# Kernel tuning notes

Measured on AMD Instinct MI355X. Metric: run time of the kernel, lower is better.

The kernel has to match this reference:

```python
import jax, jax.numpy as jnp
import numpy as np

D_MODEL = 1024
M = 64            # oscillators; state dim N = 2*M
N = 2 * M
N_H = 2           # Householder reflections per step
DT = 0.1
OMEGA_MAX = 100.0
BATCH, SEQ = 8, 2048


def setup_inputs() -> dict:
    key = jax.random.key(0)
    ks = jax.random.split(key, 8)
    u = jax.random.normal(ks[0], (BATCH, SEQ, D_MODEL), jnp.float32)
    # learned parameters (scaled like the module's small-gain init)
    W_A = jax.random.normal(ks[1], (M, D_MODEL), jnp.float32) * 0.01
    b_A = jnp.zeros((M,), jnp.float32)
    W_k = jax.random.normal(ks[2], (N_H, N, D_MODEL), jnp.float32) * 0.02
    b_k = jnp.zeros((N_H, N), jnp.float32)
    W_beta = jax.random.normal(ks[3], (N_H, D_MODEL), jnp.float32) * 0.02
    b_beta = jnp.zeros((N_H,), jnp.float32)
    B_w = jax.random.normal(ks[4], (N, D_MODEL), jnp.float32) * 0.02
    B_b = jnp.zeros((N,), jnp.float32)
    C = jax.random.normal(ks[5], (D_MODEL, N), jnp.float32) * 0.01
    D = jax.random.normal(ks[6], (D_MODEL,), jnp.float32) * 0.01
    return dict(u=u, W_A=W_A, b_A=b_A, W_k=W_k, b_k=b_k,
                W_beta=W_beta, b_beta=b_beta, B_w=B_w, B_b=B_b, C=C, D=D)


def reference(u, W_A, b_A, W_k, b_k, W_beta, b_beta, B_w, B_b, C, D):
    batch = u.shape[0]
    # --- precompute all input-dependent per-step quantities as big GEMMs ---
    A = jax.nn.relu(jnp.einsum('btd,md->btm', u, W_A) + b_A)
    A = jnp.minimum(A, OMEGA_MAX)                       # clamp(max=omega_max)
    S = 1.0 / (1.0 + (DT * DT) * A)                     # (B,T,M)
    K = jnp.einsum('btd,jnd->btjn', u, W_k) + b_k       # (B,T,n_h,N)
    K = K / jnp.maximum(jnp.linalg.norm(K, axis=-1, keepdims=True), 1e-12)
    beta = 2.0 * jax.nn.sigmoid(jnp.einsum('btd,jd->btj', u, W_beta) + b_beta)
    Bt = jnp.einsum('btd,nd->btn', u, B_w) + B_b        # (B,T,N)

    # time-major for scan
    xs = (jnp.moveaxis(A, 1, 0), jnp.moveaxis(S, 1, 0), jnp.moveaxis(K, 1, 0),
          jnp.moveaxis(beta, 1, 0), jnp.moveaxis(Bt, 1, 0))
    h0 = jnp.zeros((batch, N), u.dtype)

    def step(h, x):
        A_t, S_t, K_t, beta_t, B_t = x
        # oscillatory rotation-contraction R_t @ h (m 2x2 blocks)
        z, y = h[:, :M], h[:, M:]
        z_new = S_t * z - DT * A_t * S_t * y
        y_new = DT * S_t * z + S_t * y
        h = jnp.concatenate([z_new, y_new], axis=-1)
        # sequential Householder product H_t @ h (fixed small n_h loop)
        for j in range(N_H):
            k = K_t[:, j]                                # (B,N), unit norm
            dot = jnp.sum(k * h, axis=-1, keepdims=True)
            h = h - beta_t[:, j:j + 1] * k * dot
        h = h + B_t
        return h, h

    _, hs = jax.lax.scan(step, h0, xs)                  # (T,B,N)
    hs = jnp.moveaxis(hs, 0, 1)                         # (B,T,N)
    return jnp.einsum('btn,dn->btd', hs, C) + u * D
```

## Files before the change

kernel.cpp:

```cpp
#include <hip/hip_runtime.h>
#include <cmath>


#define NTOK 16384
#define TT 2048
#define BB 8
#define DM 1024
#define FS 520
#define CH 32
#define LCH 64
#define NW 448
#define NWP 512

typedef short bf16x8 __attribute__((ext_vector_type(8)));
typedef float f32x4 __attribute__((ext_vector_type(4)));

#define GLOAD_LDS16(g, l)                                          \
  __builtin_amdgcn_global_load_lds(                                \
      (const __attribute__((address_space(1))) void*)(g),          \
      (__attribute__((address_space(3))) void*)(l), 16, 0, 0)

__global__ __launch_bounds__(256) void packW(
    const float* __restrict__ W_A, const float* __restrict__ b_A,
    const float* __restrict__ W_k, const float* __restrict__ b_k,
    const float* __restrict__ b_beta,
    const float* __restrict__ B_w, const float* __restrict__ B_b,
    float* __restrict__ Wp, float* __restrict__ bias) {
  int r = blockIdx.x;
  int tid = threadIdx.x;
  const float* src;
  float bv;
  if (r < 64)       { src = W_A + (size_t)r * DM;         bv = b_A[r]; }
  else if (r < 320) { src = W_k + (size_t)(r - 64) * DM;  bv = b_k[r - 64]; }
  else              { src = B_w + (size_t)(r - 320) * DM; bv = B_b[r - 320]; }
  ((float4*)(Wp + (size_t)r * DM))[tid] = ((const float4*)src)[tid];
  if (tid == 0) bias[r] = bv;
  if (r == 0 && tid < 2) bias[448 + tid] = b_beta[tid];
}

__global__ __launch_bounds__(256) void transK(
    const float* __restrict__ src, float* __restrict__ dst, int M, int N) {
  __shared__ float tile[64][68];
  const int m0 = blockIdx.x * 64, n0 = blockIdx.y * 64;
  const int tid = threadIdx.x;
#pragma unroll
  for (int l = 0; l < 4; ++l) {
    int idx = tid + l * 256;
    int r = idx >> 4, c4 = (idx & 15) * 4;
    float4 v = *(const float4*)(src + (size_t)(m0 + r) * N + n0 + c4);
    tile[r][c4 + 0] = v.x; tile[r][c4 + 1] = v.y;
    tile[r][c4 + 2] = v.z; tile[r][c4 + 3] = v.w;
  }
  __syncthreads();
#pragma unroll
  for (int l = 0; l < 4; ++l) {
    int idx = tid + l * 256;
    int c = idx >> 4, r4 = (idx & 15) * 4;
    float4 w = make_float4(tile[r4 + 0][c], tile[r4 + 1][c],
                           tile[r4 + 2][c], tile[r4 + 3][c]);
    *(float4*)(dst + (size_t)(n0 + c) * M + m0 + r4) = w;
  }
}

__device__ inline unsigned short bf16_rne(float x) {
  unsigned b = __float_as_uint(x);
  b += 0x7FFFu + ((b >> 16) & 1u);
  return (unsigned short)(b >> 16);
}

__device__ inline void split_bf16(float x, unsigned short& h, unsigned short& l) {
  unsigned b = __float_as_uint(x);
  h = (unsigned short)(b >> 16);
  float rem = x - __uint_as_float(b & 0xFFFF0000u);
  l = bf16_rne(rem);
}

__global__ __launch_bounds__(256) void convertU(
    const float* __restrict__ u, unsigned short* __restrict__ uh,
    unsigned short* __restrict__ ul) {
  int gid = blockIdx.x * 256 + threadIdx.x;
  int m = gid >> 8;
  int g = gid & 255;
  float4 v = *(const float4*)(u + (size_t)m * DM + g * 4);
  int kt = g >> 3, gg = g & 7;
  int p = gg & 3, h = gg >> 2;
  int mr = m & 127, mb = m >> 7;
  int pp = p ^ ((mr >> 2) & 3);
  size_t dst = ((size_t)(mb * 32 + kt)) * 4096 + mr * 32 + ((pp << 1) | h) * 4;
  ushort4 hi, lo;
  split_bf16(v.x, hi.x, lo.x);
  split_bf16(v.y, hi.y, lo.y);
  split_bf16(v.z, hi.z, lo.z);
  split_bf16(v.w, hi.w, lo.w);
  *(ushort4*)(uh + dst) = hi;
  *(ushort4*)(ul + dst) = lo;
}

__global__ __launch_bounds__(256) void convertW(
    const float* __restrict__ Wp, unsigned short* __restrict__ Wb) {
  int gid = blockIdx.x * 256 + threadIdx.x;
  int n = gid >> 8, g = gid & 255;
  int kt = g >> 3, gg = g & 7;
  int p = gg & 3, h = gg >> 2;
  int nr = n & 127, nb = n >> 7;
  int pp = p ^ ((nr >> 2) & 3);
  size_t dst = ((size_t)(nb * 32 + kt)) * 4096 + nr * 32 + ((pp << 1) | h) * 4;
  ushort4 hv = make_ushort4(0, 0, 0, 0);
  if (n < NW) {
    float4 v = *(const float4*)(Wp + (size_t)n * DM + g * 4);
    hv.x = bf16_rne(v.x); hv.y = bf16_rne(v.y);
    hv.z = bf16_rne(v.z); hv.w = bf16_rne(v.w);
  }
  *(ushort4*)(Wb + dst) = hv;
}

__global__ __launch_bounds__(256) void convertC(
    const float* __restrict__ Cm, unsigned short* __restrict__ Chp,
    unsigned short* __restrict__ Clp) {
  int gid = blockIdx.x * 256 + threadIdx.x;
  int d = gid >> 5;
  int g = gid & 31;
  float4 v = *(const float4*)(Cm + (size_t)d * 128 + g * 4);
  int kt = g >> 3, gg = g & 7;
  int p = gg & 3, h = gg >> 2;
  int nr = d & 127, nb = d >> 7;
  int pp = p ^ ((nr >> 2) & 3);
  size_t dst = ((size_t)(nb * 4 + kt)) * 4096 + nr * 32 + ((pp << 1) | h) * 4;
  ushort4 hi, lo;
  split_bf16(v.x, hi.x, lo.x);
  split_bf16(v.y, hi.y, lo.y);
  split_bf16(v.z, hi.z, lo.z);
  split_bf16(v.w, hi.w, lo.w);
  *(ushort4*)(Chp + dst) = hi;
  *(ushort4*)(Clp + dst) = lo;
}

__global__ __launch_bounds__(256) void gemmA_mfma(
    const unsigned short* __restrict__ uh, const unsigned short* __restrict__ ul,
    const unsigned short* __restrict__ Wb, float* __restrict__ Feat, int npass) {
  __shared__ __align__(16) unsigned short As[4096];
  __shared__ __align__(16) unsigned short Bs[4096];
  const int tid = threadIdx.x;
  const int wv = tid >> 6, ln = tid & 63;
  const int lr = ln & 15, G = ln >> 4;
  const int wm = wv >> 1, wn = wv & 1;
  const int x = G ^ (lr >> 2);
  f32x4 acc[4][4];
#pragma unroll
  for (int i = 0; i < 4; ++i)
#pragma unroll
    for (int j = 0; j < 4; ++j) acc[i][j] = (f32x4){0.f, 0.f, 0.f, 0.f};

  const size_t aBase = (size_t)blockIdx.x * 32 * 4096;
  const size_t bBase = (size_t)blockIdx.y * 32 * 4096;
  const int so = wv * 512 + ln * 8;
  const int ld = wv * 512;

  for (int pass = 0; pass < npass; ++pass) {
    const unsigned short* ua = pass ? ul : uh;
    for (int kt = 0; kt < 32; ++kt) {
      const unsigned short* ga = ua + aBase + (size_t)kt * 4096;
      const unsigned short* gb = Wb + bBase + (size_t)kt * 4096;
      GLOAD_LDS16(ga + so,        As + ld);
      GLOAD_LDS16(ga + 2048 + so, As + 2048 + ld);
      GLOAD_LDS16(gb + so,        Bs + ld);
      GLOAD_LDS16(gb + 2048 + so, Bs + 2048 + ld);
      __syncthreads();
      bf16x8 af[4], bfr[4];
      const char* Ab = (const char*)As + ((wm * 64 + lr) << 6) + (x << 4);
      const char* Bb = (const char*)Bs + ((wn * 64 + lr) << 6) + (x << 4);
#pragma unroll
      for (int i = 0; i < 4; ++i) {
        af[i]  = *(const bf16x8*)(Ab + i * 1024);
        bfr[i] = *(const bf16x8*)(Bb + i * 1024);
      }
#pragma unroll
      for (int i = 0; i < 4; ++i)
#pragma unroll
        for (int j = 0; j < 4; ++j)
          acc[i][j] = __builtin_amdgcn_mfma_f32_16x16x32_bf16(
              af[i], bfr[j], acc[i][j], 0, 0, 0);
      __syncthreads();
    }
  }
  const int row0 = (blockIdx.x << 7) + wm * 64 + (G << 2);
  const int col0 = (blockIdx.y << 7) + wn * 64 + lr;
  float* fb = Feat + (size_t)row0 * FS + col0;
#pragma unroll
  for (int i = 0; i < 4; ++i)
#pragma unroll
    for (int j = 0; j < 4; ++j) {
      float* d = fb + (size_t)(i * 16) * FS + j * 16;
#pragma unroll
      for (int r = 0; r < 4; ++r) d[(size_t)r * FS] = acc[i][j][r];
    }
}

__global__ __launch_bounds__(256) void gemmC_mfma(
    const unsigned short* __restrict__ hsh, const unsigned short* __restrict__ hsl,
    const unsigned short* __restrict__ Chp, const unsigned short* __restrict__ Clp,
    const float* __restrict__ u, const float* __restrict__ Dv,
    float* __restrict__ out) {
  __shared__ __align__(16) unsigned short As[4096];
  __shared__ __align__(16) unsigned short Bs[4096];
  const int tid = threadIdx.x;
  const int wv = tid >> 6, ln = tid & 63;
  const int lr = ln & 15, G = ln >> 4;
  const int wm = wv >> 1, wn = wv & 1;
  const int x = G ^ (lr >> 2);
  f32x4 acc[4][4];
#pragma unroll
  for (int i = 0; i < 4; ++i)
#pragma unroll
    for (int j = 0; j < 4; ++j) acc[i][j] = (f32x4){0.f, 0.f, 0.f, 0.f};

  const size_t aBase = (size_t)blockIdx.x * 4 * 4096;
  const size_t bBase = (size_t)blockIdx.y * 4 * 4096;
  const int so = wv * 512 + ln * 8;
  const int ld = wv * 512;

#pragma unroll 1
  for (int pass = 0; pass < 3; ++pass) {
    const unsigned short* pa = (pass == 1) ? hsl : hsh;
    const unsigned short* pb = (pass == 2) ? Clp : Chp;
#pragma unroll 1
    for (int kt = 0; kt < 4; ++kt) {
      const unsigned short* ga = pa + aBase + (size_t)kt * 4096;
      const unsigned short* gb = pb + bBase + (size_t)kt * 4096;
      GLOAD_LDS16(ga + so,        As + ld);
      GLOAD_LDS16(ga + 2048 + so, As + 2048 + ld);
      GLOAD_LDS16(gb + so,        Bs + ld);
      GLOAD_LDS16(gb + 2048 + so, Bs + 2048 + ld);
      __syncthreads();
      bf16x8 af[4], bfr[4];
      const char* Ab = (const char*)As + ((wm * 64 + lr) << 6) + (x << 4);
      const char* Bb = (const char*)Bs + ((wn * 64 + lr) << 6) + (x << 4);
#pragma unroll
      for (int i = 0; i < 4; ++i) {
        af[i]  = *(const bf16x8*)(Ab + i * 1024);
        bfr[i] = *(const bf16x8*)(Bb + i * 1024);
      }
#pragma unroll
      for (int i = 0; i < 4; ++i)
#pragma unroll
        for (int j = 0; j < 4; ++j)
          acc[i][j] = __builtin_amdgcn_mfma_f32_16x16x32_bf16(
              af[i], bfr[j], acc[i][j], 0, 0, 0);
      __syncthreads();
    }
  }
  const int row0 = (blockIdx.x << 7) + wm * 64 + (G << 2);
  const int col0 = (blockIdx.y << 7) + wn * 64 + lr;
#pragma unroll
  for (int j = 0; j < 4; ++j) {
    float dv = Dv[col0 + j * 16];
#pragma unroll
    for (int i = 0; i < 4; ++i) {
#pragma unroll
      for (int r = 0; r < 4; ++r) {
        size_t off = (size_t)(row0 + i * 16 + r) * DM + col0 + j * 16;
        out[off] = fmaf(u[off], dv, acc[i][j][r]);
      }
    }
  }
}

__global__ __launch_bounds__(256) void gemmA_f32(
    const float* __restrict__ u, const float* __restrict__ WpT,
    float* __restrict__ Feat) {
  __shared__ float us2[128][36];
  __shared__ float wsm[32][68];
  const int tid = threadIdx.x;
  const int tx = tid & 15, ty = tid >> 4;
  const int m0 = blockIdx.x * 128;
  const int n0 = blockIdx.y * 64;
  float acc[8][4];
#pragma unroll
  for (int i = 0; i < 8; ++i)
#pragma unroll
    for (int j = 0; j < 4; ++j) acc[i][j] = 0.f;

  for (int k0 = 0; k0 < DM; k0 += 32) {
#pragma unroll
    for (int l = 0; l < 4; ++l) {
      int idx = tid + l * 256;
      int r = idx >> 3, c4 = (idx & 7) * 4;
      float4 v = *(const float4*)(u + (size_t)(m0 + r) * DM + k0 + c4);
      *(float4*)&us2[r][c4] = v;
    }
#pragma unroll
    for (int l = 0; l < 2; ++l) {
      int idx = tid + l * 256;
      int k = idx >> 4, c4 = (idx & 15) * 4;
      float4 v = *(const float4*)(WpT + (size_t)(k0 + k) * NW + n0 + c4);
      *(float4*)&wsm[k][c4] = v;
    }
    __syncthreads();
#pragma unroll
    for (int k4 = 0; k4 < 8; ++k4) {
      float4 bq0 = *(const float4*)&wsm[4 * k4 + 0][tx * 4];
      float4 bq1 = *(const float4*)&wsm[4 * k4 + 1][tx * 4];
      float4 bq2 = *(const float4*)&wsm[4 * k4 + 2][tx * 4];
      float4 bq3 = *(const float4*)&wsm[4 * k4 + 3][tx * 4];
#pragma unroll
      for (int i = 0; i < 8; ++i) {
        float4 a = *(const float4*)&us2[ty * 8 + i][4 * k4];
        acc[i][0] = fmaf(a.x, bq0.x, acc[i][0]);
        acc[i][1] = fmaf(a.x, bq0.y, acc[i][1]);
        acc[i][2] = fmaf(a.x, bq0.z, acc[i][2]);
        acc[i][3] = fmaf(a.x, bq0.w, acc[i][3]);
        acc[i][0] = fmaf(a.y, bq1.x, acc[i][0]);
        acc[i][1] = fmaf(a.y, bq1.y, acc[i][1]);
        acc[i][2] = fmaf(a.y, bq1.z, acc[i][2]);
        acc[i][3] = fmaf(a.y, bq1.w, acc[i][3]);
        acc[i][0] = fmaf(a.z, bq2.x, acc[i][0]);
        acc[i][1] = fmaf(a.z, bq2.y, acc[i][1]);
        acc[i][2] = fmaf(a.z, bq2.z, acc[i][2]);
        acc[i][3] = fmaf(a.z, bq2.w, acc[i][3]);
        acc[i][0] = fmaf(a.w, bq3.x, acc[i][0]);
        acc[i][1] = fmaf(a.w, bq3.y, acc[i][1]);
        acc[i][2] = fmaf(a.w, bq3.z, acc[i][2]);
        acc[i][3] = fmaf(a.w, bq3.w, acc[i][3]);
      }
    }
    __syncthreads();
  }
#pragma unroll
  for (int i = 0; i < 8; ++i) {
    float4 v = make_float4(acc[i][0], acc[i][1], acc[i][2], acc[i][3]);
    *(float4*)(Feat + (size_t)(m0 + ty * 8 + i) * FS + n0 + tx * 4) = v;
  }
}

__device__ inline float wave_sum(float v) {
#pragma unroll
  for (int off = 32; off > 0; off >>= 1) v += __shfl_xor(v, off, 64);
  return v;
}

__global__ __launch_bounds__(64) void postA(float* __restrict__ Feat,
                                            const float* __restrict__ bias,
                                            const float* __restrict__ u,
                                            const float* __restrict__ Wb) {
  const int t = blockIdx.x, lane = threadIdx.x;
  float* f = Feat + (size_t)t * FS;
  float s0 = 0.f, s1 = 0.f;
#pragma unroll
  for (int j = 0; j < 4; ++j) {
    float4 uv = *(const float4*)(u + (size_t)t * DM + j * 256 + lane * 4);
    float4 w0 = *(const float4*)(Wb + j * 256 + lane * 4);
    float4 w1 = *(const float4*)(Wb + DM + j * 256 + lane * 4);
    s0 = fmaf(uv.x, w0.x, s0); s0 = fmaf(uv.y, w0.y, s0);
    s0 = fmaf(uv.z, w0.z, s0); s0 = fmaf(uv.w, w0.w, s0);
    s1 = fmaf(uv.x, w1.x, s1); s1 = fmaf(uv.y, w1.y, s1);
    s1 = fmaf(uv.z, w1.z, s1); s1 = fmaf(uv.w, w1.w, s1);
  }
  s0 = wave_sum(s0); s1 = wave_sum(s1);
  float a = f[lane] + bias[lane];
  a = fminf(fmaxf(a, 0.f), 100.f);
  float S = 1.f / (1.f + 0.01f * a);
  f[lane] = S;
  f[448 + lane] = 0.1f * a * S;
  float k10 = f[64 + lane] + bias[64 + lane];
  float k11 = f[128 + lane] + bias[128 + lane];
  float n1 = wave_sum(k10 * k10 + k11 * k11);
  float inv1 = 1.f / fmaxf(sqrtf(n1), 1e-12f);
  k10 *= inv1; k11 *= inv1;
  f[64 + lane] = k10; f[128 + lane] = k11;
  float k20 = f[192 + lane] + bias[192 + lane];
  float k21 = f[256 + lane] + bias[256 + lane];
  float n2 = wave_sum(k20 * k20 + k21 * k21);
  float inv2 = 1.f / fmaxf(sqrtf(n2), 1e-12f);
  k20 *= inv2; k21 *= inv2;
  f[192 + lane] = k20; f[256 + lane] = k21;
  float c12 = wave_sum(k10 * k20 + k11 * k21);
  if (lane == 0) {
    f[512] = 2.f / (1.f + expf(-(s0 + bias[448])));
    f[513] = 2.f / (1.f + expf(-(s1 + bias[449])));
    f[514] = c12;
  }
  f[320 + lane] += bias[320 + lane];
  f[384 + lane] += bias[384 + lane];
}

__global__ __launch_bounds__(512, 2) void scanB1(
    const float* __restrict__ Feat, float* __restrict__ Mc) {
  const int cid = blockIdx.x;
  const int t0 = (cid >> 5) * TT + (cid & 31) * LCH;
  const int tid = threadIdx.x;
  const int col = tid >> 2, q = tid & 3;
  const int i0 = q * 16;
  __shared__ float fb[2][4 * FS];
  float mz[16], my[16];
#pragma unroll
  for (int j = 0; j < 16; ++j) {
    mz[j] = (i0 + j == col) ? 1.f : 0.f;
    my[j] = (64 + i0 + j == col) ? 1.f : 0.f;
  }
  {
    const float4* src = (const float4*)(Feat + (size_t)t0 * FS);
    for (int v = tid; v < FS; v += 512) ((float4*)fb[0])[v] = src[v];
  }
  __syncthreads();
  for (int g = 0; g < 16; ++g) {
    const int cur = g & 1;
    float4 pf0, pf1;
    const bool has2 = tid < (FS - 512);
    if (g < 15) {
      const float4* src = (const float4*)(Feat + (size_t)(t0 + (g + 1) * 4) * FS);
      pf0 = src[tid];
      if (has2) pf1 = src[tid + 512];
    }
#pragma unroll
    for (int s = 0; s < 4; ++s) {
      const float* f = fb[cur] + s * FS;
      float sj[16], cj[16], k1z[16], k1y[16], k2z[16], k2y[16];
#pragma unroll
      for (int v = 0; v < 4; ++v) {
        *(float4*)&sj[4 * v]  = *(const float4*)(f + i0 + 4 * v);
        *(float4*)&cj[4 * v]  = *(const float4*)(f + 448 + i0 + 4 * v);
        *(float4*)&k1z[4 * v] = *(const float4*)(f + 64 + i0 + 4 * v);
        *(float4*)&k1y[4 * v] = *(const float4*)(f + 128 + i0 + 4 * v);
        *(float4*)&k2z[4 * v] = *(const float4*)(f + 192 + i0 + 4 * v);
        *(float4*)&k2y[4 * v] = *(const float4*)(f + 256 + i0 + 4 * v);
      }
      float4 sc = *(const float4*)(f + 512);
      float p = 0.f, r2 = 0.f;
#pragma unroll
      for (int j = 0; j < 16; ++j) {
        float s0 = sj[j], c1 = cj[j];
        float z = mz[j], y = my[j];
        float sz = s0 * z;
        z = fmaf(-c1, y, sz);
        y = fmaf(s0, y, 0.1f * sz);
        mz[j] = z; my[j] = y;
        p  = fmaf(k1z[j], z, p);  p  = fmaf(k1y[j], y, p);
        r2 = fmaf(k2z[j], z, r2); r2 = fmaf(k2y[j], y, r2);
      }
      p  += __shfl_xor(p, 1, 64);  p  += __shfl_xor(p, 2, 64);
      r2 += __shfl_xor(r2, 1, 64); r2 += __shfl_xor(r2, 2, 64);
      float e1 = sc.x * p;
      float e2 = sc.y * fmaf(-sc.z, e1, r2);
#pragma unroll
      for (int j = 0; j < 16; ++j) {
        float z = fmaf(-e1, k1z[j], mz[j]);
        mz[j] = fmaf(-e2, k2z[j], z);
        float y = fmaf(-e1, k1y[j], my[j]);
        my[j] = fmaf(-e2, k2y[j], y);
      }
    }
    if (g < 15) {
      ((float4*)fb[1 - cur])[tid] = pf0;
      if (has2) ((float4*)fb[1 - cur])[tid + 512] = pf1;
    }
    __syncthreads();
  }
  float* dst = Mc + ((size_t)cid * 128 + col) * 128;
#pragma unroll
  for (int v = 0; v < 4; ++v)
    *(float4*)(dst + i0 + 4 * v) = *(float4*)&mz[4 * v];
#pragma unroll
  for (int v = 0; v < 4; ++v)
    *(float4*)(dst + 64 + i0 + 4 * v) = *(float4*)&my[4 * v];
}

__global__ __launch_bounds__(64) void scanB0(
    const float* __restrict__ Feat, float* __restrict__ dc) {
  const int cid = blockIdx.x;
  const int lane = threadIdx.x;
  float z = 0.f, y = 0.f;
  const int t0 = (cid >> 5) * TT + (cid & 31) * LCH;
  for (int t = t0; t < t0 + LCH; ++t) {
    const float* __restrict__ f = Feat + (size_t)t * FS;
    float s = f[lane], c1 = f[448 + lane];
    float k1z = f[64 + lane], k1y = f[128 + lane];
    float k2z = f[192 + lane], k2y = f[256 + lane];
    float bz = f[320 + lane], by = f[384 + lane];
    float b1 = f[512], b2 = f[513], c12 = f[514];
    float sz = s * z;
    float zn = fmaf(-c1, y, sz);
    float yn = fmaf(s, y, 0.1f * sz);
    float p = fmaf(k1y, yn, k1z * zn);
    float qq = fmaf(k2y, yn, k2z * zn);
#pragma unroll
    for (int off = 32; off > 0; off >>= 1) {
      p += __shfl_xor(p, off, 64);
      qq += __shfl_xor(qq, off, 64);
    }
    float e1 = b1 * p;
    float d2 = fmaf(-c12, e1, qq);
    float e2 = b2 * d2;
    z = fmaf(-e1, k1z, zn); z = fmaf(-e2, k2z, z); z += bz;
    y = fmaf(-e1, k1y, yn); y = fmaf(-e2, k2y, y); y += by;
  }
  dc[(size_t)cid * 128 + lane] = z;
  dc[(size_t)cid * 128 + 64 + lane] = y;
}

__global__ __launch_bounds__(256) void scanB2(
    const float* __restrict__ Mc, const float* __restrict__ dc,
    float* __restrict__ hstart) {
  const int b = blockIdx.x;
  const int tid = threadIdx.x;
  const int i = tid & 127, jh = tid >> 7;
  __shared__ float h[128];
  __shared__ float red[2][128];
  if (tid < 128) h[tid] = 0.f;
  __syncthreads();
  float mreg[64];
  {
    const float* M0 = Mc + (size_t)(b * CH) * 16384;
#pragma unroll
    for (int j = 0; j < 64; ++j) mreg[j] = M0[(size_t)(jh * 64 + j) * 128 + i];
  }
  for (int c = 0; c < CH; ++c) {
    if (tid < 128) hstart[(size_t)(b * CH + c) * 128 + tid] = h[tid];
    float acc = 0.f;
#pragma unroll
    for (int j = 0; j < 64; ++j) acc = fmaf(mreg[j], h[jh * 64 + j], acc);
    red[jh][i] = acc;
    if (c + 1 < CH) {
      const float* Mn = Mc + (size_t)(b * CH + c + 1) * 16384;
#pragma unroll
      for (int j = 0; j < 64; ++j) mreg[j] = Mn[(size_t)(jh * 64 + j) * 128 + i];
    }
    __syncthreads();
    if (tid < 128)
      h[tid] = red[0][tid] + red[1][tid] + dc[(size_t)(b * CH + c) * 128 + tid];
    __syncthreads();
  }
}

__global__ __launch_bounds__(64) void scanB3(
    const float* __restrict__ Feat, const float* __restrict__ hstart,
    float* __restrict__ hs, unsigned short* __restrict__ hsh,
    unsigned short* __restrict__ hsl, int split) {
  const int cid = blockIdx.x;
  const int lane = threadIdx.x;
  float z = hstart[(size_t)cid * 128 + lane];
  float y = hstart[(size_t)cid * 128 + 64 + lane];
  const int t0 = (cid >> 5) * TT + (cid & 31) * LCH;
  const int ktz = lane >> 5, kkz = lane & 31;
  const int kty = (64 + lane) >> 5, kky = lane & 31;
  const int pz = (kkz >> 2) & 3, hz = kkz >> 4;
  const int lowz = kkz & 3;
  for (int t = t0; t < t0 + LCH; ++t) {
    const float* __restrict__ f = Feat + (size_t)t * FS;
    float s = f[lane], c1 = f[448 + lane];
    float k1z = f[64 + lane], k1y = f[128 + lane];
    float k2z = f[192 + lane], k2y = f[256 + lane];
    float bz = f[320 + lane], by = f[384 + lane];
    float b1 = f[512], b2 = f[513], c12 = f[514];
    float sz = s * z;
    float zn = fmaf(-c1, y, sz);
    float yn = fmaf(s, y, 0.1f * sz);
    float p = fmaf(k1y, yn, k1z * zn);
    float qq = fmaf(k2y, yn, k2z * zn);
#pragma unroll
    for (int off = 32; off > 0; off >>= 1) {
      p += __shfl_xor(p, off, 64);
      qq += __shfl_xor(qq, off, 64);
    }
    float e1 = b1 * p;
    float d2 = fmaf(-c12, e1, qq);
    float e2 = b2 * d2;
    zn = fmaf(-e1, k1z, zn); zn = fmaf(-e2, k2z, zn); zn += bz;
    yn = fmaf(-e1, k1y, yn); yn = fmaf(-e2, k2y, yn); yn += by;
    if (split) {
      const int mb = t >> 7, mr = t & 127;
      const int xr = (mr >> 2) & 3;
      {
        size_t idx = ((size_t)(mb * 4 + ktz)) * 4096 + mr * 32 +
                     ((((pz ^ xr) << 1) | hz)) * 4 + lowz;
        unsigned short hi, lo;
        split_bf16(zn, hi, lo);
        hsh[idx] = hi; hsl[idx] = lo;
      }
      {
        size_t idx = ((size_t)(mb * 4 + kty)) * 4096 + mr * 32 +
                     ((((pz ^ xr) << 1) | hz)) * 4 + lowz;
        unsigned short hi, lo;
        split_bf16(yn, hi, lo);
        hsh[idx] = hi; hsl[idx] = lo;
      }
    } else {
      hs[(size_t)t * 128 + lane] = zn;
      hs[(size_t)t * 128 + 64 + lane] = yn;
    }
    z = zn; y = yn;
  }
  (void)kky;
}

__global__ __launch_bounds__(256) void gemmC(
    const float* __restrict__ hs, const float* __restrict__ CmT,
    const float* __restrict__ u, const float* __restrict__ Dv,
    float* __restrict__ out) {
  __shared__ float as2[64][68];
  __shared__ float bs[64][68];
  const int tid = threadIdx.x;
  const int tx = tid & 15, ty = tid >> 4;
  const int t0 = blockIdx.x * 64;
  const int d0 = blockIdx.y * 64;
  float acc[4][4];
#pragma unroll
  for (int i = 0; i < 4; ++i)
#pragma unroll
    for (int j = 0; j < 4; ++j) acc[i][j] = 0.f;

  for (int kb = 0; kb < 128; kb += 64) {
#pragma unroll
    for (int l = 0; l < 4; ++l) {
      int idx = tid + l * 256;
      int r = idx >> 4, c4 = (idx & 15) * 4;
      float4 v = *(const float4*)(hs + (size_t)(t0 + r) * 128 + kb + c4);
      *(float4*)&as2[r][c4] = v;
      float4 w = *(const float4*)(CmT + (size_t)(kb + r) * DM + d0 + c4);
      *(float4*)&bs[r][c4] = w;
    }
    __syncthreads();
#pragma unroll
    for (int k4 = 0; k4 < 16; ++k4) {
      float4 bq0 = *(const float4*)&bs[4 * k4 + 0][tx * 4];
      float4 bq1 = *(const float4*)&bs[4 * k4 + 1][tx * 4];
      float4 bq2 = *(const float4*)&bs[4 * k4 + 2][tx * 4];
      float4 bq3 = *(const float4*)&bs[4 * k4 + 3][tx * 4];
#pragma unroll
      for (int i = 0; i < 4; ++i) {
        float4 a = *(const float4*)&as2[ty * 4 + i][4 * k4];
        acc[i][0] = fmaf(a.x, bq0.x, acc[i][0]);
        acc[i][1] = fmaf(a.x, bq0.y, acc[i][1]);
        acc[i][2] = fmaf(a.x, bq0.z, acc[i][2]);
        acc[i][3] = fmaf(a.x, bq0.w, acc[i][3]);
        acc[i][0] = fmaf(a.y, bq1.x, acc[i][0]);
        acc[i][1] = fmaf(a.y, bq1.y, acc[i][1]);
        acc[i][2] = fmaf(a.y, bq1.z, acc[i][2]);
        acc[i][3] = fmaf(a.y, bq1.w, acc[i][3]);
        acc[i][0] = fmaf(a.z, bq2.x, acc[i][0]);
        acc[i][1] = fmaf(a.z, bq2.y, acc[i][1]);
        acc[i][2] = fmaf(a.z, bq2.z, acc[i][2]);
        acc[i][3] = fmaf(a.z, bq2.w, acc[i][3]);
        acc[i][0] = fmaf(a.w, bq3.x, acc[i][0]);
        acc[i][1] = fmaf(a.w, bq3.y, acc[i][1]);
        acc[i][2] = fmaf(a.w, bq3.z, acc[i][2]);
        acc[i][3] = fmaf(a.w, bq3.w, acc[i][3]);
      }
    }
    __syncthreads();
  }
#pragma unroll
  for (int i = 0; i < 4; ++i) {
    int row = t0 + ty * 4 + i;
    float4 uv = *(const float4*)(u + (size_t)row * DM + d0 + tx * 4);
    float4 dv = *(const float4*)(Dv + d0 + tx * 4);
    float4 o;
    o.x = fmaf(uv.x, dv.x, acc[i][0]);
    o.y = fmaf(uv.y, dv.y, acc[i][1]);
    o.z = fmaf(uv.z, dv.z, acc[i][2]);
    o.w = fmaf(uv.w, dv.w, acc[i][3]);
    *(float4*)(out + (size_t)row * DM + d0 + tx * 4) = o;
  }
}

extern "C" void kernel_launch(void* const* d_in, const int* in_sizes, int n_in,
                              void* d_out, int out_size, void* d_ws, size_t ws_size,
                              hipStream_t stream) {
  const float* u      = (const float*)d_in[0];
  const float* W_A    = (const float*)d_in[1];
  const float* b_A    = (const float*)d_in[2];
  const float* W_k    = (const float*)d_in[3];
  const float* b_k    = (const float*)d_in[4];
  const float* W_beta = (const float*)d_in[5];
  const float* b_beta = (const float*)d_in[6];
  const float* B_w    = (const float*)d_in[7];
  const float* B_b    = (const float*)d_in[8];
  const float* Cm     = (const float*)d_in[9];
  const float* Dv     = (const float*)d_in[10];
  float* out = (float*)d_out;
  char* ws = (char*)d_ws;
  float* Wp     = (float*)(ws);
  float* WpT    = (float*)(ws + 1835008);
  unsigned short* Wb = (unsigned short*)(ws + 1835008);
  float* CmT    = (float*)(ws + 3670016);
  float* bias   = (float*)(ws + 4194304);
  float* Feat   = (float*)(ws + 4198400);
  float* Mc     = (float*)(ws + 38277120);
  float* dcv    = (float*)(ws + 55054336);
  float* hstart = (float*)(ws + 55185408);
  float* hsb    = (float*)(ws + 55316480);
  unsigned short* uh = (unsigned short*)(ws + 38277120);
  unsigned short* ul = (unsigned short*)(ws + 71831552);
  unsigned short* hsh = (unsigned short*)(ws + 71831552);
  unsigned short* hsl = (unsigned short*)(ws + 76025856);
  unsigned short* Chp = (unsigned short*)(ws + 80220160);
  unsigned short* Clp = (unsigned short*)(ws + 80482304);
  const size_t NEED1 = 71831552;
  const size_t NEED2 = 105385984;

  packW<<<dim3(448), dim3(256), 0, stream>>>(W_A, b_A, W_k, b_k, b_beta,
                                             B_w, B_b, Wp, bias);
  transK<<<dim3(16, 2), dim3(256), 0, stream>>>(Cm, CmT, DM, 128);

  const bool big1 = (ws_size == 0) || (ws_size >= NEED1);
  const bool big2 = (ws_size == 0) || (ws_size >= NEED2);
  if (big1) {
    const int npass = big2 ? 2 : 1;
    convertW<<<dim3(512), dim3(256), 0, stream>>>(Wp, Wb);
    convertU<<<dim3(16384), dim3(256), 0, stream>>>(u, uh, big2 ? ul : uh);
    gemmA_mfma<<<dim3(128, 4), dim3(256), 0, stream>>>(uh, ul, Wb, Feat, npass);
    if (big2)
      convertC<<<dim3(128), dim3(256), 0, stream>>>(Cm, Chp, Clp);
  } else {
    transK<<<dim3(7, 16), dim3(256), 0, stream>>>(Wp, WpT, NW, DM);
    gemmA_f32<<<dim3(128, 7), dim3(256), 0, stream>>>(u, WpT, Feat);
  }
  postA<<<dim3(16384), dim3(64), 0, stream>>>(Feat, bias, u, W_beta);
  scanB1<<<dim3(256), dim3(512), 0, stream>>>(Feat, Mc);
  scanB0<<<dim3(256), dim3(64), 0, stream>>>(Feat, dcv);
  scanB2<<<dim3(8), dim3(256), 0, stream>>>(Mc, dcv, hstart);
  if (big2) {
    scanB3<<<dim3(256), dim3(64), 0, stream>>>(Feat, hstart, hsb, hsh, hsl, 1);
    gemmC_mfma<<<dim3(128, 8), dim3(256), 0, stream>>>(hsh, hsl, Chp, Clp,
                                                       u, Dv, out);
  } else {
    scanB3<<<dim3(256), dim3(64), 0, stream>>>(Feat, hstart, hsb, hsh, hsl, 0);
    gemmC<<<dim3(256, 16), dim3(256), 0, stream>>>(hsb, CmT, u, Dv, out);
  }
}
```

Measured before the change: 423.3 us.

## Double-buffer MFMA GEMM loads and halve scan chunk length with wider blocks

Both MFMA GEMMs now prefetch the next K tile into a second LDS buffer while computing the current one, so each iteration waits on one barrier instead of two. The chunked scan switches to 512 chunks of 32 steps each. This shortens the sequential phases in scanB1, scanB0 and scanB3, at the cost of a longer 64-step carry chain in scanB2. scanB1 and scanB2 move to 1024-thread blocks with more parallel partial sums. The fp32 fallback path, transK and the workspace-size checks are removed, so the code now assumes a large workspace is always available.

```diff
diff --git a/kernel.cpp b/kernel.cpp
--- a/kernel.cpp
+++ b/kernel.cpp
@@ -7,8 +7,9 @@
 #define BB 8
 #define DM 1024
 #define FS 520
-#define CH 32
-#define LCH 64
+#define CH 64
+#define LCH 32
+#define NCH 512
 #define NW 448
 #define NWP 512
 
@@ -36,30 +37,6 @@
   ((float4*)(Wp + (size_t)r * DM))[tid] = ((const float4*)src)[tid];
   if (tid == 0) bias[r] = bv;
   if (r == 0 && tid < 2) bias[448 + tid] = b_beta[tid];
-}
-
-__global__ __launch_bounds__(256) void transK(
-    const float* __restrict__ src, float* __restrict__ dst, int M, int N) {
-  __shared__ float tile[64][68];
-  const int m0 = blockIdx.x * 64, n0 = blockIdx.y * 64;
-  const int tid = threadIdx.x;
-#pragma unroll
-  for (int l = 0; l < 4; ++l) {
-    int idx = tid + l * 256;
-    int r = idx >> 4, c4 = (idx & 15) * 4;
-    float4 v = *(const float4*)(src + (size_t)(m0 + r) * N + n0 + c4);
-    tile[r][c4 + 0] = v.x; tile[r][c4 + 1] = v.y;
-    tile[r][c4 + 2] = v.z; tile[r][c4 + 3] = v.w;
-  }
-  __syncthreads();
-#pragma unroll
-  for (int l = 0; l < 4; ++l) {
-    int idx = tid + l * 256;
-    int c = idx >> 4, r4 = (idx & 15) * 4;
-    float4 w = make_float4(tile[r4 + 0][c], tile[r4 + 1][c],
-                           tile[r4 + 2][c], tile[r4 + 3][c]);
-    *(float4*)(dst + (size_t)(n0 + c) * M + m0 + r4) = w;
-  }
 }
 
 __device__ inline unsigned short bf16_rne(float x) {
@@ -137,9 +114,9 @@
 
 __global__ __launch_bounds__(256) void gemmA_mfma(
     const unsigned short* __restrict__ uh, const unsigned short* __restrict__ ul,
-    const unsigned short* __restrict__ Wb, float* __restrict__ Feat, int npass) {
-  __shared__ __align__(16) unsigned short As[4096];
-  __shared__ __align__(16) unsigned short Bs[4096];
+    const unsigned short* __restrict__ Wb, float* __restrict__ Feat) {
+  __shared__ __align__(16) unsigned short As[8192];
+  __shared__ __align__(16) unsigned short Bs[8192];
   const int tid = threadIdx.x;
   const int wv = tid >> 6, ln = tid & 63;
   const int lr = ln & 15, G = ln >> 4;
@@ -156,32 +133,39 @@
   const int so = wv * 512 + ln * 8;
   const int ld = wv * 512;
 
-  for (int pass = 0; pass < npass; ++pass) {
-    const unsigned short* ua = pass ? ul : uh;
-    for (int kt = 0; kt < 32; ++kt) {
-      const unsigned short* ga = ua + aBase + (size_t)kt * 4096;
-      const unsigned short* gb = Wb + bBase + (size_t)kt * 4096;
-      GLOAD_LDS16(ga + so,        As + ld);
-      GLOAD_LDS16(ga + 2048 + so, As + 2048 + ld);
-      GLOAD_LDS16(gb + so,        Bs + ld);
-      GLOAD_LDS16(gb + 2048 + so, Bs + 2048 + ld);
-      __syncthreads();
-      bf16x8 af[4], bfr[4];
-      const char* Ab = (const char*)As + ((wm * 64 + lr) << 6) + (x << 4);
-      const char* Bb = (const char*)Bs + ((wn * 64 + lr) << 6) + (x << 4);
-#pragma unroll
-      for (int i = 0; i < 4; ++i) {
-        af[i]  = *(const bf16x8*)(Ab + i * 1024);
-        bfr[i] = *(const bf16x8*)(Bb + i * 1024);
-      }
-#pragma unroll
-      for (int i = 0; i < 4; ++i)
-#pragma unroll
-        for (int j = 0; j < 4; ++j)
-          acc[i][j] = __builtin_amdgcn_mfma_f32_16x16x32_bf16(
-              af[i], bfr[j], acc[i][j], 0, 0, 0);
-      __syncthreads();
-    }
+  auto stage = [&](int step, int buf) {
+    const unsigned short* pa = (step < 32) ? uh : ul;
+    const int kt = step & 31;
+    const unsigned short* ga = pa + aBase + (size_t)kt * 4096;
+    const unsigned short* gb = Wb + bBase + (size_t)kt * 4096;
+    unsigned short* A = As + buf * 4096;
+    unsigned short* B = Bs + buf * 4096;
+    GLOAD_LDS16(ga + so,        A + ld);
+    GLOAD_LDS16(ga + 2048 + so, A + 2048 + ld);
+    GLOAD_LDS16(gb + so,        B + ld);
+    GLOAD_LDS16(gb + 2048 + so, B + 2048 + ld);
+  };
+
+  stage(0, 0);
+  __syncthreads();
+  for (int s = 0; s < 64; ++s) {
+    const int cur = s & 1;
+    if (s + 1 < 64) stage(s + 1, cur ^ 1);
+    bf16x8 af[4], bfr[4];
+    const char* Ab = (const char*)(As + cur * 4096) + ((wm * 64 + lr) << 6) + (x << 4);
+    const char* Bb = (const char*)(Bs + cur * 4096) + ((wn * 64 + lr) << 6) + (x << 4);
+#pragma unroll
+    for (int i = 0; i < 4; ++i) {
+      af[i]  = *(const bf16x8*)(Ab + i * 1024);
+      bfr[i] = *(const bf16x8*)(Bb + i * 1024);
+    }
+#pragma unroll
+    for (int i = 0; i < 4; ++i)
+#pragma unroll
+      for (int j = 0; j < 4; ++j)
+        acc[i][j] = __builtin_amdgcn_mfma_f32_16x16x32_bf16(
+            af[i], bfr[j], acc[i][j], 0, 0, 0);
+    __syncthreads();
   }
   const int row0 = (blockIdx.x << 7) + wm * 64 + (G << 2);
   const int col0 = (blockIdx.y << 7) + wn * 64 + lr;
@@ -201,8 +185,8 @@
     const unsigned short* __restrict__ Chp, const unsigned short* __restrict__ Clp,
     const float* __restrict__ u, const float* __restrict__ Dv,
     float* __restrict__ out) {
-  __shared__ __align__(16) unsigned short As[4096];
-  __shared__ __align__(16) unsigned short Bs[4096];
+  __shared__ __align__(16) unsigned short As[8192];
+  __shared__ __align__(16) unsigned short Bs[8192];
   const int tid = threadIdx.x;
   const int wv = tid >> 6, ln = tid & 63;
   const int lr = ln & 15, G = ln >> 4;
@@ -219,35 +203,40 @@
   const int so = wv * 512 + ln * 8;
   const int ld = wv * 512;
 
-#pragma unroll 1
-  for (int pass = 0; pass < 3; ++pass) {
+  auto stage = [&](int step, int buf) {
+    const int pass = step >> 2, kt = step & 3;
     const unsigned short* pa = (pass == 1) ? hsl : hsh;
     const unsigned short* pb = (pass == 2) ? Clp : Chp;
-#pragma unroll 1
-    for (int kt = 0; kt < 4; ++kt) {
-      const unsigned short* ga = pa + aBase + (size_t)kt * 4096;
-      const unsigned short* gb = pb + bBase + (size_t)kt * 4096;
-      GLOAD_LDS16(ga + so,        As + ld);
-      GLOAD_LDS16(ga + 2048 + so, As + 2048 + ld);
-      GLOAD_LDS16(gb + so,        Bs + ld);
-      GLOAD_LDS16(gb + 2048 + so, Bs + 2048 + ld);
-      __syncthreads();
-      bf16x8 af[4], bfr[4];
-      const char* Ab = (const char*)As + ((wm * 64 + lr) << 6) + (x << 4);
-      const char* Bb = (const char*)Bs + ((wn * 64 + lr) << 6) + (x << 4);
-#pragma unroll
-      for (int i = 0; i < 4; ++i) {
-        af[i]  = *(const bf16x8*)(Ab + i * 1024);
-        bfr[i] = *(const bf16x8*)(Bb + i * 1024);
-      }
-#pragma unroll
-      for (int i = 0; i < 4; ++i)
-#pragma unroll
-        for (int j = 0; j < 4; ++j)
-          acc[i][j] = __builtin_amdgcn_mfma_f32_16x16x32_bf16(
-              af[i], bfr[j], acc[i][j], 0, 0, 0);
-      __syncthreads();
-    }
+    const unsigned short* ga = pa + aBase + (size_t)kt * 4096;
+    const unsigned short* gb = pb + bBase + (size_t)kt * 4096;
+    unsigned short* A = As + buf * 4096;
+    unsigned short* B = Bs + buf * 4096;
+    GLOAD_LDS16(ga + so,        A + ld);
+    GLOAD_LDS16(ga + 2048 + so, A + 2048 + ld);
+    GLOAD_LDS16(gb + so,        B + ld);
+    GLOAD_LDS16(gb + 2048 + so, B + 2048 + ld);
+  };
+
+  stage(0, 0);
+  __syncthreads();
+  for (int s = 0; s < 12; ++s) {
+    const int cur = s & 1;
+    if (s + 1 < 12) stage(s + 1, cur ^ 1);
+    bf16x8 af[4], bfr[4];
+    const char* Ab = (const char*)(As + cur * 4096) + ((wm * 64 + lr) << 6) + (x << 4);
+    const char* Bb = (const char*)(Bs + cur * 4096) + ((wn * 64 + lr) << 6) + (x << 4);
+#pragma unroll
+    for (int i = 0; i < 4; ++i) {
+      af[i]  = *(const bf16x8*)(Ab + i * 1024);
+      bfr[i] = *(const bf16x8*)(Bb + i * 1024);
+    }
+#pragma unroll
+    for (int i = 0; i < 4; ++i)
+#pragma unroll
+      for (int j = 0; j < 4; ++j)
+        acc[i][j] = __builtin_amdgcn_mfma_f32_16x16x32_bf16(
+            af[i], bfr[j], acc[i][j], 0, 0, 0);
+    __syncthreads();
   }
   const int row0 = (blockIdx.x << 7) + wm * 64 + (G << 2);
   const int col0 = (blockIdx.y << 7) + wn * 64 + lr;
@@ -262,73 +251,6 @@
         out[off] = fmaf(u[off], dv, acc[i][j][r]);
       }
     }
-  }
-}
-
-__global__ __launch_bounds__(256) void gemmA_f32(
-    const float* __restrict__ u, const float* __restrict__ WpT,
-    float* __restrict__ Feat) {
-  __shared__ float us2[128][36];
-  __shared__ float wsm[32][68];
-  const int tid = threadIdx.x;
-  const int tx = tid & 15, ty = tid >> 4;
-  const int m0 = blockIdx.x * 128;
-  const int n0 = blockIdx.y * 64;
-  float acc[8][4];
-#pragma unroll
-  for (int i = 0; i < 8; ++i)
-#pragma unroll
-    for (int j = 0; j < 4; ++j) acc[i][j] = 0.f;
-
-  for (int k0 = 0; k0 < DM; k0 += 32) {
-#pragma unroll
-    for (int l = 0; l < 4; ++l) {
-      int idx = tid + l * 256;
-      int r = idx >> 3, c4 = (idx & 7) * 4;
-      float4 v = *(const float4*)(u + (size_t)(m0 + r) * DM + k0 + c4);
-      *(float4*)&us2[r][c4] = v;
-    }
-#pragma unroll
-    for (int l = 0; l < 2; ++l) {
-      int idx = tid + l * 256;
-      int k = idx >> 4, c4 = (idx & 15) * 4;
-      float4 v = *(const float4*)(WpT + (size_t)(k0 + k) * NW + n0 + c4);
-      *(float4*)&wsm[k][c4] = v;
-    }
-    __syncthreads();
-#pragma unroll
-    for (int k4 = 0; k4 < 8; ++k4) {
-      float4 bq0 = *(const float4*)&wsm[4 * k4 + 0][tx * 4];
-      float4 bq1 = *(const float4*)&wsm[4 * k4 + 1][tx * 4];
-      float4 bq2 = *(const float4*)&wsm[4 * k4 + 2][tx * 4];
-      float4 bq3 = *(const float4*)&wsm[4 * k4 + 3][tx * 4];
-#pragma unroll
-      for (int i = 0; i < 8; ++i) {
-        float4 a = *(const float4*)&us2[ty * 8 + i][4 * k4];
-        acc[i][0] = fmaf(a.x, bq0.x, acc[i][0]);
-        acc[i][1] = fmaf(a.x, bq0.y, acc[i][1]);
-        acc[i][2] = fmaf(a.x, bq0.z, acc[i][2]);
-        acc[i][3] = fmaf(a.x, bq0.w, acc[i][3]);
-        acc[i][0] = fmaf(a.y, bq1.x, acc[i][0]);
-        acc[i][1] = fmaf(a.y, bq1.y, acc[i][1]);
-        acc[i][2] = fmaf(a.y, bq1.z, acc[i][2]);
-        acc[i][3] = fmaf(a.y, bq1.w, acc[i][3]);
-        acc[i][0] = fmaf(a.z, bq2.x, acc[i][0]);
-        acc[i][1] = fmaf(a.z, bq2.y, acc[i][1]);
-        acc[i][2] = fmaf(a.z, bq2.z, acc[i][2]);
-        acc[i][3] = fmaf(a.z, bq2.w, acc[i][3]);
-        acc[i][0] = fmaf(a.w, bq3.x, acc[i][0]);
-        acc[i][1] = fmaf(a.w, bq3.y, acc[i][1]);
-        acc[i][2] = fmaf(a.w, bq3.z, acc[i][2]);
-        acc[i][3] = fmaf(a.w, bq3.w, acc[i][3]);
-      }
-    }
-    __syncthreads();
-  }
-#pragma unroll
-  for (int i = 0; i < 8; ++i) {
-    float4 v = make_float4(acc[i][0], acc[i][1], acc[i][2], acc[i][3]);
-    *(float4*)(Feat + (size_t)(m0 + ty * 8 + i) * FS + n0 + tx * 4) = v;
   }
 }
 
@@ -383,40 +305,39 @@
   f[384 + lane] += bias[384 + lane];
 }
 
-__global__ __launch_bounds__(512, 2) void scanB1(
+__global__ __launch_bounds__(1024, 8) void scanB1(
     const float* __restrict__ Feat, float* __restrict__ Mc) {
   const int cid = blockIdx.x;
-  const int t0 = (cid >> 5) * TT + (cid & 31) * LCH;
+  const int t0 = (cid >> 6) * TT + (cid & 63) * LCH;
   const int tid = threadIdx.x;
-  const int col = tid >> 2, q = tid & 3;
-  const int i0 = q * 16;
+  const int col = tid >> 3, q = tid & 7;
+  const int i0 = q * 8;
   __shared__ float fb[2][4 * FS];
-  float mz[16], my[16];
-#pragma unroll
-  for (int j = 0; j < 16; ++j) {
+  float mz[8], my[8];
+#pragma unroll
+  for (int j = 0; j < 8; ++j) {
     mz[j] = (i0 + j == col) ? 1.f : 0.f;
     my[j] = (64 + i0 + j == col) ? 1.f : 0.f;
   }
   {
     const float4* src = (const float4*)(Feat + (size_t)t0 * FS);
-    for (int v = tid; v < FS; v += 512) ((float4*)fb[0])[v] = src[v];
+    if (tid < FS) ((float4*)fb[0])[tid] = src[tid];
   }
   __syncthreads();
-  for (int g = 0; g < 16; ++g) {
+  for (int g = 0; g < LCH / 4; ++g) {
     const int cur = g & 1;
-    float4 pf0, pf1;
-    const bool has2 = tid < (FS - 512);
-    if (g < 15) {
+    float4 pf0;
+    const bool pre = (g < LCH / 4 - 1) && (tid < FS);
+    if (pre) {
       const float4* src = (const float4*)(Feat + (size_t)(t0 + (g + 1) * 4) * FS);
       pf0 = src[tid];
-      if (has2) pf1 = src[tid + 512];
     }
 #pragma unroll
     for (int s = 0; s < 4; ++s) {
       const float* f = fb[cur] + s * FS;
-      float sj[16], cj[16], k1z[16], k1y[16], k2z[16], k2y[16];
-#pragma unroll
-      for (int v = 0; v < 4; ++v) {
+      float sj[8], cj[8], k1z[8], k1y[8], k2z[8], k2y[8];
+#pragma unroll
+      for (int v = 0; v < 2; ++v) {
         *(float4*)&sj[4 * v]  = *(const float4*)(f + i0 + 4 * v);
         *(float4*)&cj[4 * v]  = *(const float4*)(f + 448 + i0 + 4 * v);
         *(float4*)&k1z[4 * v] = *(const float4*)(f + 64 + i0 + 4 * v);
@@ -425,43 +346,46 @@
         *(float4*)&k2y[4 * v] = *(const float4*)(f + 256 + i0 + 4 * v);
       }
       float4 sc = *(const float4*)(f + 512);
-      float p = 0.f, r2 = 0.f;
-#pragma unroll
-      for (int j = 0; j < 16; ++j) {
+      float p0 = 0.f, p1 = 0.f, r0 = 0.f, r1 = 0.f;
+#pragma unroll
+      for (int j = 0; j < 8; ++j) {
         float s0 = sj[j], c1 = cj[j];
         float z = mz[j], y = my[j];
         float sz = s0 * z;
         z = fmaf(-c1, y, sz);
         y = fmaf(s0, y, 0.1f * sz);
         mz[j] = z; my[j] = y;
-        p  = fmaf(k1z[j], z, p);  p  = fmaf(k1y[j], y, p);
-        r2 = fmaf(k2z[j], z, r2); r2 = fmaf(k2y[j], y, r2);
+        if (j & 1) {
+          p1 = fmaf(k1z[j], z, p1); p1 = fmaf(k1y[j], y, p1);
+          r1 = fmaf(k2z[j], z, r1); r1 = fmaf(k2y[j], y, r1);
+        } else {
+          p0 = fmaf(k1z[j], z, p0); p0 = fmaf(k1y[j], y, p0);
+          r0 = fmaf(k2z[j], z, r0); r0 = fmaf(k2y[j], y, r0);
+        }
       }
+      float p = p0 + p1, r2 = r0 + r1;
       p  += __shfl_xor(p, 1, 64);  p  += __shfl_xor(p, 2, 64);
+      p  += __shfl_xor(p, 4, 64);
       r2 += __shfl_xor(r2, 1, 64); r2 += __shfl_xor(r2, 2, 64);
+      r2 += __shfl_xor(r2, 4, 64);
       float e1 = sc.x * p;
       float e2 = sc.y * fmaf(-sc.z, e1, r2);
 #pragma unroll
-      for (int j = 0; j < 16; ++j) {
+      for (int j = 0; j < 8; ++j) {
         float z = fmaf(-e1, k1z[j], mz[j]);
         mz[j] = fmaf(-e2, k2z[j], z);
         float y = fmaf(-e1, k1y[j], my[j]);
         my[j] = fmaf(-e2, k2y[j], y);
       }
     }
-    if (g < 15) {
-      ((float4*)fb[1 - cur])[tid] = pf0;
-      if (has2) ((float4*)fb[1 - cur])[tid + 512] = pf1;
-    }
+    if (pre) ((float4*)fb[1 - cur])[tid] = pf0;
     __syncthreads();
   }
   float* dst = Mc + ((size_t)cid * 128 + col) * 128;
-#pragma unroll
-  for (int v = 0; v < 4; ++v)
-    *(float4*)(dst + i0 + 4 * v) = *(float4*)&mz[4 * v];
-#pragma unroll
-  for (int v = 0; v < 4; ++v)
-    *(float4*)(dst + 64 + i0 + 4 * v) = *(float4*)&my[4 * v];
+  *(float4*)(dst + i0)          = *(float4*)&mz[0];
+  *(float4*)(dst + i0 + 4)      = *(float4*)&mz[4];
+  *(float4*)(dst + 64 + i0)     = *(float4*)&my[0];
+  *(float4*)(dst + 64 + i0 + 4) = *(float4*)&my[4];
 }
 
 __global__ __launch_bounds__(64) void scanB0(
@@ -469,7 +393,7 @@
   const int cid = blockIdx.x;
   const int lane = threadIdx.x;
   float z = 0.f, y = 0.f;
-  const int t0 = (cid >> 5) * TT + (cid & 31) * LCH;
+  const int t0 = (cid >> 6) * TT + (cid & 63) * LCH;
   for (int t = t0; t < t0 + LCH; ++t) {
     const float* __restrict__ f = Feat + (size_t)t * FS;
     float s = f[lane], c1 = f[448 + lane];
@@ -497,51 +421,54 @@
   dc[(size_t)cid * 128 + 64 + lane] = y;
 }
 
-__global__ __launch_bounds__(256) void scanB2(
+__global__ __launch_bounds__(1024, 8) void scanB2(
     const float* __restrict__ Mc, const float* __restrict__ dc,
     float* __restrict__ hstart) {
   const int b = blockIdx.x;
   const int tid = threadIdx.x;
   const int i = tid & 127, jh = tid >> 7;
   __shared__ float h[128];
-  __shared__ float red[2][128];
+  __shared__ float red[8][128];
   if (tid < 128) h[tid] = 0.f;
   __syncthreads();
-  float mreg[64];
+  float mreg[16];
   {
     const float* M0 = Mc + (size_t)(b * CH) * 16384;
 #pragma unroll
-    for (int j = 0; j < 64; ++j) mreg[j] = M0[(size_t)(jh * 64 + j) * 128 + i];
+    for (int j = 0; j < 16; ++j) mreg[j] = M0[(size_t)(jh * 16 + j) * 128 + i];
   }
   for (int c = 0; c < CH; ++c) {
     if (tid < 128) hstart[(size_t)(b * CH + c) * 128 + tid] = h[tid];
     float acc = 0.f;
 #pragma unroll
-    for (int j = 0; j < 64; ++j) acc = fmaf(mreg[j], h[jh * 64 + j], acc);
+    for (int j = 0; j < 16; ++j) acc = fmaf(mreg[j], h[jh * 16 + j], acc);
     red[jh][i] = acc;
     if (c + 1 < CH) {
       const float* Mn = Mc + (size_t)(b * CH + c + 1) * 16384;
 #pragma unroll
-      for (int j = 0; j < 64; ++j) mreg[j] = Mn[(size_t)(jh * 64 + j) * 128 + i];
+      for (int j = 0; j < 16; ++j) mreg[j] = Mn[(size_t)(jh * 16 + j) * 128 + i];
     }
     __syncthreads();
-    if (tid < 128)
-      h[tid] = red[0][tid] + red[1][tid] + dc[(size_t)(b * CH + c) * 128 + tid];
+    if (tid < 128) {
+      float sum = dc[(size_t)(b * CH + c) * 128 + tid];
+#pragma unroll
+      for (int k = 0; k < 8; ++k) sum += red[k][tid];
+      h[tid] = sum;
+    }
     __syncthreads();
   }
 }
 
 __global__ __launch_bounds__(64) void scanB3(
     const float* __restrict__ Feat, const float* __restrict__ hstart,
-    float* __restrict__ hs, unsigned short* __restrict__ hsh,
-    unsigned short* __restrict__ hsl, int split) {
+    unsigned short* __restrict__ hsh, unsigned short* __restrict__ hsl) {
   const int cid = blockIdx.x;
   const int lane = threadIdx.x;
   float z = hstart[(size_t)cid * 128 + lane];
   float y = hstart[(size_t)cid * 128 + 64 + lane];
-  const int t0 = (cid >> 5) * TT + (cid & 31) * LCH;
+  const int t0 = (cid >> 6) * TT + (cid & 63) * LCH;
   const int ktz = lane >> 5, kkz = lane & 31;
-  const int kty = (64 + lane) >> 5, kky = lane & 31;
+  const int kty = (64 + lane) >> 5;
   const int pz = (kkz >> 2) & 3, hz = kkz >> 4;
   const int lowz = kkz & 3;
   for (int t = t0; t < t0 + LCH; ++t) {
@@ -566,99 +493,20 @@
     float e2 = b2 * d2;
     zn = fmaf(-e1, k1z, zn); zn = fmaf(-e2, k2z, zn); zn += bz;
     yn = fmaf(-e1, k1y, yn); yn = fmaf(-e2, k2y, yn); yn += by;
-    if (split) {
+    {
       const int mb = t >> 7, mr = t & 127;
       const int xr = (mr >> 2) & 3;
-      {
-        size_t idx = ((size_t)(mb * 4 + ktz)) * 4096 + mr * 32 +
-                     ((((pz ^ xr) << 1) | hz)) * 4 + lowz;
-        unsigned short hi, lo;
-        split_bf16(zn, hi, lo);
-        hsh[idx] = hi; hsl[idx] = lo;
-      }
-      {
-        size_t idx = ((size_t)(mb * 4 + kty)) * 4096 + mr * 32 +
-                     ((((pz ^ xr) << 1) | hz)) * 4 + lowz;
-        unsigned short hi, lo;
-        split_bf16(yn, hi, lo);
-        hsh[idx] = hi; hsl[idx] = lo;
-      }
-    } else {
-      hs[(size_t)t * 128 + lane] = zn;
-      hs[(size_t)t * 128 + 64 + lane] = yn;
+      size_t idxz = ((size_t)(mb * 4 + ktz)) * 4096 + mr * 32 +
+                    ((((pz ^ xr) << 1) | hz)) * 4 + lowz;
+      size_t idxy = ((size_t)(mb * 4 + kty)) * 4096 + mr * 32 +
+                    ((((pz ^ xr) << 1) | hz)) * 4 + lowz;
+      unsigned short hi, lo;
+      split_bf16(zn, hi, lo);
+      hsh[idxz] = hi; hsl[idxz] = lo;
+      split_bf16(yn, hi, lo);
+      hsh[idxy] = hi; hsl[idxy] = lo;
     }
     z = zn; y = yn;
-  }
-  (void)kky;
-}
-
-__global__ __launch_bounds__(256) void gemmC(
-    const float* __restrict__ hs, const float* __restrict__ CmT,
-    const float* __restrict__ u, const float* __restrict__ Dv,
-    float* __restrict__ out) {
-  __shared__ float as2[64][68];
-  __shared__ float bs[64][68];
-  const int tid = threadIdx.x;
-  const int tx = tid & 15, ty = tid >> 4;
-  const int t0 = blockIdx.x * 64;
-  const int d0 = blockIdx.y * 64;
-  float acc[4][4];
-#pragma unroll
-  for (int i = 0; i < 4; ++i)
-#pragma unroll
-    for (int j = 0; j < 4; ++j) acc[i][j] = 0.f;
-
-  for (int kb = 0; kb < 128; kb += 64) {
-#pragma unroll
-    for (int l = 0; l < 4; ++l) {
-      int idx = tid + l * 256;
-      int r = idx >> 4, c4 = (idx & 15) * 4;
-      float4 v = *(const float4*)(hs + (size_t)(t0 + r) * 128 + kb + c4);
-      *(float4*)&as2[r][c4] = v;
-      float4 w = *(const float4*)(CmT + (size_t)(kb + r) * DM + d0 + c4);
-      *(float4*)&bs[r][c4] = w;
-    }
-    __syncthreads();
-#pragma unroll
-    for (int k4 = 0; k4 < 16; ++k4) {
-      float4 bq0 = *(const float4*)&bs[4 * k4 + 0][tx * 4];
-      float4 bq1 = *(const float4*)&bs[4 * k4 + 1][tx * 4];
-      float4 bq2 = *(const float4*)&bs[4 * k4 + 2][tx * 4];
-      float4 bq3 = *(const float4*)&bs[4 * k4 + 3][tx * 4];
-#pragma unroll
-      for (int i = 0; i < 4; ++i) {
-        float4 a = *(const float4*)&as2[ty * 4 + i][4 * k4];
-        acc[i][0] = fmaf(a.x, bq0.x, acc[i][0]);
-        acc[i][1] = fmaf(a.x, bq0.y, acc[i][1]);
-        acc[i][2] = fmaf(a.x, bq0.z, acc[i][2]);
-        acc[i][3] = fmaf(a.x, bq0.w, acc[i][3]);
-        acc[i][0] = fmaf(a.y, bq1.x, acc[i][0]);
-        acc[i][1] = fmaf(a.y, bq1.y, acc[i][1]);
-        acc[i][2] = fmaf(a.y, bq1.z, acc[i][2]);
-        acc[i][3] = fmaf(a.y, bq1.w, acc[i][3]);
-        acc[i][0] = fmaf(a.z, bq2.x, acc[i][0]);
-        acc[i][1] = fmaf(a.z, bq2.y, acc[i][1]);
-        acc[i][2] = fmaf(a.z, bq2.z, acc[i][2]);
-        acc[i][3] = fmaf(a.z, bq2.w, acc[i][3]);
-        acc[i][0] = fmaf(a.w, bq3.x, acc[i][0]);
-        acc[i][1] = fmaf(a.w, bq3.y, acc[i][1]);
-        acc[i][2] = fmaf(a.w, bq3.z, acc[i][2]);
-        acc[i][3] = fmaf(a.w, bq3.w, acc[i][3]);
-      }
-    }
-    __syncthreads();
-  }
-#pragma unroll
-  for (int i = 0; i < 4; ++i) {
-    int row = t0 + ty * 4 + i;
-    float4 uv = *(const float4*)(u + (size_t)row * DM + d0 + tx * 4);
-    float4 dv = *(const float4*)(Dv + d0 + tx * 4);
-    float4 o;
-    o.x = fmaf(uv.x, dv.x, acc[i][0]);
-    o.y = fmaf(uv.y, dv.y, acc[i][1]);
-    o.z = fmaf(uv.z, dv.z, acc[i][2]);
-    o.w = fmaf(uv.w, dv.w, acc[i][3]);
-    *(float4*)(out + (size_t)row * DM + d0 + tx * 4) = o;
   }
 }
 
@@ -679,51 +527,30 @@
   float* out = (float*)d_out;
   char* ws = (char*)d_ws;
   float* Wp     = (float*)(ws);
-  float* WpT    = (float*)(ws + 1835008);
   unsigned short* Wb = (unsigned short*)(ws + 1835008);
-  float* CmT    = (float*)(ws + 3670016);
   float* bias   = (float*)(ws + 4194304);
   float* Feat   = (float*)(ws + 4198400);
+  unsigned short* uh = (unsigned short*)(ws + 38277120);
   float* Mc     = (float*)(ws + 38277120);
-  float* dcv    = (float*)(ws + 55054336);
-  float* hstart = (float*)(ws + 55185408);
-  float* hsb    = (float*)(ws + 55316480);
-  unsigned short* uh = (unsigned short*)(ws + 38277120);
   unsigned short* ul = (unsigned short*)(ws + 71831552);
   unsigned short* hsh = (unsigned short*)(ws + 71831552);
   unsigned short* hsl = (unsigned short*)(ws + 76025856);
   unsigned short* Chp = (unsigned short*)(ws + 80220160);
   unsigned short* Clp = (unsigned short*)(ws + 80482304);
-  const size_t NEED1 = 71831552;
-  const size_t NEED2 = 105385984;
+  float* dcv    = (float*)(ws + 80744448);
+  float* hstart = (float*)(ws + 81006592);
 
   packW<<<dim3(448), dim3(256), 0, stream>>>(W_A, b_A, W_k, b_k, b_beta,
                                              B_w, B_b, Wp, bias);
-  transK<<<dim3(16, 2), dim3(256), 0, stream>>>(Cm, CmT, DM, 128);
-
-  const bool big1 = (ws_size == 0) || (ws_size >= NEED1);
-  const bool big2 = (ws_size == 0) || (ws_size >= NEED2);
-  if (big1) {
-    const int npass = big2 ? 2 : 1;
-    convertW<<<dim3(512), dim3(256), 0, stream>>>(Wp, Wb);
-    convertU<<<dim3(16384), dim3(256), 0, stream>>>(u, uh, big2 ? ul : uh);
-    gemmA_mfma<<<dim3(128, 4), dim3(256), 0, stream>>>(uh, ul, Wb, Feat, npass);
-    if (big2)
-      convertC<<<dim3(128), dim3(256), 0, stream>>>(Cm, Chp, Clp);
-  } else {
-    transK<<<dim3(7, 16), dim3(256), 0, stream>>>(Wp, WpT, NW, DM);
-    gemmA_f32<<<dim3(128, 7), dim3(256), 0, stream>>>(u, WpT, Feat);
-  }
+  convertW<<<dim3(512), dim3(256), 0, stream>>>(Wp, Wb);
+  convertU<<<dim3(16384), dim3(256), 0, stream>>>(u, uh, ul);
+  gemmA_mfma<<<dim3(128, 4), dim3(256), 0, stream>>>(uh, ul, Wb, Feat);
+  convertC<<<dim3(128), dim3(256), 0, stream>>>(Cm, Chp, Clp);
   postA<<<dim3(16384), dim3(64), 0, stream>>>(Feat, bias, u, W_beta);
-  scanB1<<<dim3(256), dim3(512), 0, stream>>>(Feat, Mc);
-  scanB0<<<dim3(256), dim3(64), 0, stream>>>(Feat, dcv);
-  scanB2<<<dim3(8), dim3(256), 0, stream>>>(Mc, dcv, hstart);
-  if (big2) {
-    scanB3<<<dim3(256), dim3(64), 0, stream>>>(Feat, hstart, hsb, hsh, hsl, 1);
-    gemmC_mfma<<<dim3(128, 8), dim3(256), 0, stream>>>(hsh, hsl, Chp, Clp,
-                                                       u, Dv, out);
-  } else {
-    scanB3<<<dim3(256), dim3(64), 0, stream>>>(Feat, hstart, hsb, hsh, hsl, 0);
-    gemmC<<<dim3(256, 16), dim3(256), 0, stream>>>(hsb, CmT, u, Dv, out);
-  }
-}
+  scanB1<<<dim3(NCH), dim3(1024), 0, stream>>>(Feat, Mc);
+  scanB0<<<dim3(NCH), dim3(64), 0, stream>>>(Feat, dcv);
+  scanB2<<<dim3(8), dim3(1024), 0, stream>>>(Mc, dcv, hstart);
+  scanB3<<<dim3(NCH), dim3(64), 0, stream>>>(Feat, hstart, hsh, hsl);
+  gemmC_mfma<<<dim3(128, 8), dim3(256), 0, stream>>>(hsh, hsl, Chp, Clp,
+                                                     u, Dv, out);
+}
```

After: 429.4 us. Within noise of the previous version (+1.4%).
